# Optimization experiments

Measured on AMD Instinct MI355X. Metric: run time of the kernel, lower is better.

## Reference

```python
import jax, jax.numpy as jnp
import numpy as np

B, S, D, H = 2, 4096, 1024, 16
DH = D // H  # 64


def setup_inputs() -> dict:
    key = jax.random.key(0)
    ks = jax.random.split(key, 5)
    x = jax.random.normal(ks[0], (B, S, D), dtype=jnp.float32)
    scale = 1.0 / np.sqrt(D)
    Wq = jax.random.normal(ks[1], (D, D), dtype=jnp.float32) * scale
    Wk = jax.random.normal(ks[2], (D, D), dtype=jnp.float32) * scale
    Wv = jax.random.normal(ks[3], (D, D), dtype=jnp.float32) * scale
    Wo = jax.random.normal(ks[4], (D, D), dtype=jnp.float32) * scale
    bo = jnp.zeros((D,), dtype=jnp.float32)
    return {"x": x, "Wq": Wq, "Wk": Wk, "Wv": Wv, "Wo": Wo, "bo": bo}


def reference(x, Wq, Wk, Wv, Wo, bo):
    b, s, d = x.shape
    # QKV projections (no bias), split heads: [b, s, H, DH]
    q = (x @ Wq).reshape(b, s, H, DH)
    k = (x @ Wk).reshape(b, s, H, DH)
    v = (x @ Wv).reshape(b, s, H, DH)
    # scores: [b, H, s, s]
    scores = jnp.einsum("bqhd,bkhd->bhqk", q, k)
    # causal mask: upper triangle (j > i) set to -inf, then scale by sqrt(d_head)
    causal = jnp.triu(jnp.ones((s, s), dtype=bool), k=1)
    scores = jnp.where(causal, -jnp.inf, scores)
    weights = jax.nn.softmax(scores / jnp.sqrt(jnp.float32(DH)), axis=-1)
    # dropout rate is 0.0 -> identity
    ctx = jnp.einsum("bhqk,bkhd->bqhd", weights, v).reshape(b, s, d)
    return ctx @ Wo + bo
```

## Files before the change

### kernel.cpp

```cpp
#include <hip/hip_runtime.h>
#include <hip/hip_bf16.h>
#include <stdint.h>
#include <math.h>

#define BATCH 2
#define S_LEN 4096
#define DMODEL 1024
#define NH 16
#define DHEAD 64
#define MTOK (BATCH * S_LEN)

#define QSCALE 0.1803368801111793f

typedef unsigned short u16;
typedef __attribute__((ext_vector_type(8))) short bf16x8;
typedef __attribute__((ext_vector_type(4))) float f32x4;
typedef __attribute__((ext_vector_type(16))) float f32x16;
typedef __attribute__((ext_vector_type(4))) unsigned short u16x4;

__device__ __forceinline__ float b2f(u16 u) {
  union { unsigned int i; float f; } v; v.i = ((unsigned int)u) << 16; return v.f;
}
__device__ __forceinline__ u16 f2b(float f) {
  union { float f; unsigned int i; } v; v.f = f;
  unsigned int r = v.i + 0x7FFF + ((v.i >> 16) & 1);
  return (u16)(r >> 16);
}
__device__ __forceinline__ unsigned int pk2(float hi, float lo) {
  union { float f; unsigned int u; } a, b; a.f = hi; b.f = lo;
  return __builtin_amdgcn_perm(a.u, b.u, 0x07060302u);
}
__device__ __forceinline__ void pswap(unsigned int& a, unsigned int& b) {
  asm("v_permlane32_swap_b32 %0, %1" : "+v"(a), "+v"(b));
}

__device__ __forceinline__ void gl_lds16(const u16* g, u16* l) {
  __builtin_amdgcn_global_load_lds(
      (__attribute__((address_space(1))) void*)(u16*)g,
      (__attribute__((address_space(3))) void*)l, 16, 0, 0);
}

__global__ void detect_dtype(const unsigned int* __restrict__ x, int* __restrict__ flag) {
  __shared__ int cnt;
  if (threadIdx.x == 0) cnt = 0;
  __syncthreads();
  int c = 0;
  for (int i = threadIdx.x; i < 4096; i += 256) {
    unsigned int w = x[i];
    int e = (w >> 7) & 0xFF;
    if (e >= 100 && e <= 135) c++;
  }
  atomicAdd(&cnt, c);
  __syncthreads();
  if (threadIdx.x == 0) *flag = (cnt > 2048) ? 1 : 0;
}

__global__ void convert_x(const void* __restrict__ xin, u16* __restrict__ xc,
                          const int* __restrict__ flagp) {
  const int isb = *flagp;
  long e = ((long)blockIdx.x * 256 + threadIdx.x) * 4;
  if (isb) {
    *(uint2*)&xc[e] = *(const uint2*)((const u16*)xin + e);
  } else {
    float4 f = *(const float4*)((const float*)xin + e);
    xc[e + 0] = f2b(f.x);
    xc[e + 1] = f2b(f.y);
    xc[e + 2] = f2b(f.z);
    xc[e + 3] = f2b(f.w);
  }
}

__global__ void transpose4(const void* __restrict__ W0, const void* __restrict__ W1,
                           const void* __restrict__ W2, const void* __restrict__ W3,
                           u16* __restrict__ out, const int* __restrict__ flagp) {
  __shared__ u16 tile[32][33];
  const int isb = *flagp;
  int z = blockIdx.z;
  const void* W = (z == 0) ? W0 : (z == 1) ? W1 : (z == 2) ? W2 : W3;
  u16* o = out + (long)z * (DMODEL * DMODEL);
  int x = blockIdx.x * 32 + threadIdx.x;
  int y0 = blockIdx.y * 32;
  if (isb) {
    const u16* Wb = (const u16*)W;
#pragma unroll
    for (int i = 0; i < 32; i += 8)
      tile[threadIdx.y + i][threadIdx.x] = Wb[(long)(y0 + threadIdx.y + i) * DMODEL + x];
  } else {
    const float* Wf = (const float*)W;
#pragma unroll
    for (int i = 0; i < 32; i += 8)
      tile[threadIdx.y + i][threadIdx.x] = f2b(Wf[(long)(y0 + threadIdx.y + i) * DMODEL + x]);
  }
  __syncthreads();
  int x2 = blockIdx.y * 32 + threadIdx.x;
  int y2 = blockIdx.x * 32;
#pragma unroll
  for (int i = 0; i < 32; i += 8)
    o[(long)(y2 + threadIdx.y + i) * DMODEL + x2] = tile[threadIdx.x][threadIdx.y + i];
}

#define BM3 128
#define BN3 256
#define BK3 32
#define NT3 (DMODEL / BK3)
#define BUF3 12288

#define VM6 asm volatile("s_waitcnt vmcnt(6)" ::: "memory")
#define VM0 asm volatile("s_waitcnt vmcnt(0)" ::: "memory")
#define BARX do { asm volatile("" ::: "memory"); __builtin_amdgcn_s_barrier(); \
                  asm volatile("" ::: "memory"); } while (0)

#define STAGE3(t_, dst_)                                                          \
  do {                                                                            \
    const u16* a_ = pA + (t_) * BK3;                                              \
    const u16* b_ = pB + (t_) * BK3;                                              \
    u16* ad_ = (dst_) + w * 1024;                                                 \
    u16* bd_ = (dst_) + 4096 + w * 2048;                                          \
    gl_lds16(a_, ad_);                                                            \
    gl_lds16(a_ + 16 * DMODEL, ad_ + 512);                                        \
    gl_lds16(b_, bd_);                                                            \
    gl_lds16(b_ + 16 * DMODEL, bd_ + 512);                                        \
    gl_lds16(b_ + 32 * DMODEL, bd_ + 1024);                                       \
    gl_lds16(b_ + 48 * DMODEL, bd_ + 1536);                                       \
  } while (0)

#define GEMM_CORE5(A_, Bt_, NX_)                                                  \
  __shared__ __align__(16) u16 lds[3 * BUF3];                                     \
  const int tid = threadIdx.x;                                                    \
  const int w = tid >> 6;                                                         \
  const int lane = tid & 63;                                                      \
  const int nwg = (int)gridDim.x;                                                 \
  const int wg = (int)blockIdx.x;                                                 \
  const int swz = (wg & 7) * (nwg >> 3) + (wg >> 3);                              \
  const int m0 = (swz / (NX_)) * BM3;                                             \
  const int n0 = (swz % (NX_)) * BN3;                                             \
  const int wn = w * 64;                                                          \
  const int lc = lane & 15;                                                       \
  const int lq = lane >> 4;                                                       \
  const u16* pA = (A_) + (long)(m0 + w * 32 + (lane >> 2)) * DMODEL + (lane & 3) * 8; \
  const u16* pB = (Bt_) + (long)(n0 + w * 64 + (lane >> 2)) * DMODEL + (lane & 3) * 8; \
  f32x4 acc[8][4] = {};                                                           \
  STAGE3(0, lds);                                                                 \
  STAGE3(1, lds + BUF3);                                                          \
  for (int t = 0; t < NT3; ++t) {                                                 \
    if (t < NT3 - 1) { VM6; } else { VM0; }                                       \
    BARX;                                                                         \
    if (t + 2 < NT3) STAGE3(t + 2, lds + ((t + 2) % 3) * BUF3);                   \
    const u16* la = lds + (t % 3) * BUF3;                                         \
    const u16* lb = la + 4096;                                                    \
    bf16x8 af[8], bg[4];                                                          \
    _Pragma("unroll")                                                             \
    for (int j = 0; j < 4; ++j)                                                   \
      bg[j] = *(const bf16x8*)&lb[(wn + j * 16 + lc) * 32 + lq * 8];              \
    _Pragma("unroll")                                                             \
    for (int i = 0; i < 8; ++i)                                                   \
      af[i] = *(const bf16x8*)&la[(i * 16 + lc) * 32 + lq * 8];                   \
    __builtin_amdgcn_s_setprio(1);                                                \
    _Pragma("unroll")                                                             \
    for (int i = 0; i < 8; ++i)                                                   \
      _Pragma("unroll")                                                           \
      for (int j = 0; j < 4; ++j)                                                 \
        acc[i][j] = __builtin_amdgcn_mfma_f32_16x16x32_bf16(af[i], bg[j], acc[i][j], 0, 0, 0); \
    __builtin_amdgcn_s_setprio(0);                                                \
  }

__global__ __launch_bounds__(256, 2)
void gemm_qkv(const u16* __restrict__ A, const u16* __restrict__ Bt,
              u16* __restrict__ Qo, u16* __restrict__ Ko, u16* __restrict__ Vo) {
  GEMM_CORE5(A, Bt, 12)
#pragma unroll
  for (int i = 0; i < 8; ++i) {
#pragma unroll
    for (int j = 0; j < 4; ++j) {
      int n = n0 + wn + j * 16 + lc;
      int rgn = n >> 10;
      int nn = n & 1023;
      int h = nn >> 6, dh = nn & (DHEAD - 1);
      int m_base = m0 + i * 16 + lq * 4;
      int b = m_base >> 12, s0q = m_base & (S_LEN - 1);
      if (rgn == 2) {
        long idx_v = (((long)(b * NH + h)) * DHEAD + dh) * S_LEN + s0q;
        u16x4 vv;
#pragma unroll
        for (int r = 0; r < 4; ++r) vv[r] = f2b(acc[i][j][r]);
        *(u16x4*)&Vo[idx_v] = vv;
      } else {
        float sc = (rgn == 0) ? QSCALE : 1.0f;
        u16* dst = (rgn == 0) ? Qo : Ko;
#pragma unroll
        for (int r = 0; r < 4; ++r) {
          long idx_r = (((long)(b * NH + h)) * S_LEN + s0q + r) * DHEAD + dh;
          dst[idx_r] = f2b(acc[i][j][r] * sc);
        }
      }
    }
  }
}

__global__ __launch_bounds__(256, 2)
void gemm_out(const u16* __restrict__ A, const u16* __restrict__ Bt,
              const void* __restrict__ bias, void* __restrict__ C,
              const int* __restrict__ flagp) {
  GEMM_CORE5(A, Bt, 4)
  const int isb = *flagp;
#pragma unroll
  for (int i = 0; i < 8; ++i) {
#pragma unroll
    for (int j = 0; j < 4; ++j) {
      int n = n0 + wn + j * 16 + lc;
      float bv = isb ? b2f(((const u16*)bias)[n]) : ((const float*)bias)[n];
#pragma unroll
      for (int r = 0; r < 4; ++r) {
        int m = m0 + i * 16 + lq * 4 + r;
        float v = acc[i][j][r] + bv;
        if (isb) ((u16*)C)[(long)m * DMODEL + n] = f2b(v);
        else     ((float*)C)[(long)m * DMODEL + n] = v;
      }
    }
  }
}

__global__ __launch_bounds__(256, 2)
void flash_attn(const u16* __restrict__ Q, const u16* __restrict__ K,
                const u16* __restrict__ Vt, u16* __restrict__ ctx) {
  __shared__ __align__(16) u16 lK[2][64 * 64];
  __shared__ __align__(16) u16 lV[2][64 * 64];

  const int tid = threadIdx.x;
  const int w = tid >> 6;
  const int lane = tid & 63;
  const int l31 = lane & 31;
  const int l5 = lane >> 5;

  const int hb = blockIdx.x;
  const int h = hb & (NH - 1);
  const int b = hb >> 4;
  const int qt = gridDim.y - 1 - (int)blockIdx.y;
  const int q0 = qt * 128;

  const int bh = b * NH + h;
  const u16* Qb = Q + (long)bh * S_LEN * DHEAD;
  const u16* Kb = K + (long)bh * S_LEN * DHEAD;
  const u16* Vb = Vt + (long)bh * DHEAD * S_LEN;

  const int qa = q0 + w * 32;
  const int myq = qa + l31;

  bf16x8 aq[4];
#pragma unroll
  for (int c = 0; c < 4; ++c)
    aq[c] = *(const bf16x8*)(Qb + (long)myq * DHEAD + c * 16 + l5 * 8);

  union OU { unsigned int wd[4]; bf16x8 v; } ones;
#pragma unroll
  for (int i = 0; i < 4; ++i) ones.wd[i] = 0x3F803F80u;

  const int srow = tid >> 2;
  const int sc0 = (tid & 3) * 2;
  const int sd0 = srow * 64 + ((sc0 ^ (srow & 7)) * 8);
  const int sd1 = srow * 64 + (((sc0 + 1) ^ (srow & 7)) * 8);
  const u16* kp = Kb + (long)srow * DHEAD + sc0 * 8;
  const u16* vp = Vb + (long)srow * S_LEN + sc0 * 8;

  const int kmax = q0 + 64;
  bf16x8 kr0 = *(const bf16x8*)kp;
  bf16x8 kr1 = *(const bf16x8*)(kp + 8);
  bf16x8 vr0 = *(const bf16x8*)vp;
  bf16x8 vr1 = *(const bf16x8*)(vp + 8);
  const u16* kpre = kp + 64 * DHEAD;
  const u16* vpre = vp + 64;

  f32x16 o0 = {}, o1 = {};
  f32x16 lacc = {};
  const int xsw = l31 & 7;

  int offK[4][2];
#pragma unroll
  for (int c = 0; c < 4; ++c) {
    const int ch = c * 2 + l5;
    offK[c][0] = l31 * 64 + ((ch ^ xsw) * 8);
    offK[c][1] = (32 + l31) * 64 + ((ch ^ xsw) * 8);
  }

  for (int k0 = 0; k0 <= kmax; k0 += 64) {
    const int bi = (k0 >> 6) & 1;
    u16* lk = lK[bi];
    u16* lv = lV[bi];
    *(bf16x8*)&lk[sd0] = kr0;
    *(bf16x8*)&lk[sd1] = kr1;
    *(bf16x8*)&lv[sd0] = vr0;
    *(bf16x8*)&lv[sd1] = vr1;
    __syncthreads();

    if (k0 + 64 <= kmax) {
      kr0 = *(const bf16x8*)kpre;
      kr1 = *(const bf16x8*)(kpre + 8);
      vr0 = *(const bf16x8*)vpre;
      vr1 = *(const bf16x8*)(vpre + 8);
      kpre += 64 * DHEAD;
      vpre += 64;
    }

    if (k0 <= qa + 31) {
      f32x16 s0 = {}, s1 = {};
      __builtin_amdgcn_s_setprio(1);
#pragma unroll
      for (int c = 0; c < 4; ++c) {
        bf16x8 ak0 = *(const bf16x8*)&lk[offK[c][0]];
        bf16x8 ak1 = *(const bf16x8*)&lk[offK[c][1]];
        s0 = __builtin_amdgcn_mfma_f32_32x32x16_bf16(ak0, aq[c], s0, 0, 0, 0);
        s1 = __builtin_amdgcn_mfma_f32_32x32x16_bf16(ak1, aq[c], s1, 0, 0, 0);
      }
      __builtin_amdgcn_s_setprio(0);

      const bool masked = (k0 + 63 > qa);
      union BPU { unsigned int wd[4]; bf16x8 v; };
      BPU bp[4];
#pragma unroll
      for (int ph = 0; ph < 2; ++ph) {
        const f32x16 sv = ph ? s1 : s0;
        float p[16];
#pragma unroll
        for (int rr = 0; rr < 16; ++rr) {
          float e = __builtin_amdgcn_exp2f(sv[rr]);
          if (masked) {
            int kv = k0 + ph * 32 + (rr & 3) + 8 * (rr >> 2) + 4 * l5;
            e = (kv > myq) ? 0.0f : e;
          }
          p[rr] = e;
        }
#pragma unroll
        for (int g = 0; g < 2; ++g) {
          unsigned int A0 = pk2(p[8 * g + 1], p[8 * g + 0]);
          unsigned int A1 = pk2(p[8 * g + 3], p[8 * g + 2]);
          unsigned int B0 = pk2(p[8 * g + 5], p[8 * g + 4]);
          unsigned int B1 = pk2(p[8 * g + 7], p[8 * g + 6]);
          pswap(A0, B0);
          pswap(A1, B1);
          const int kc = ph * 2 + g;
          bp[kc].wd[0] = A0; bp[kc].wd[1] = A1;
          bp[kc].wd[2] = B0; bp[kc].wd[3] = B1;
        }
      }

      __builtin_amdgcn_s_setprio(1);
#pragma unroll
      for (int kc = 0; kc < 4; ++kc) {
        bf16x8 av0 = *(const bf16x8*)&lv[offK[kc][0]];
        bf16x8 av1 = *(const bf16x8*)&lv[offK[kc][1]];
        o0 = __builtin_amdgcn_mfma_f32_32x32x16_bf16(av0, bp[kc].v, o0, 0, 0, 0);
        o1 = __builtin_amdgcn_mfma_f32_32x32x16_bf16(av1, bp[kc].v, o1, 0, 0, 0);
        lacc = __builtin_amdgcn_mfma_f32_32x32x16_bf16(ones.v, bp[kc].v, lacc, 0, 0, 0);
      }
      __builtin_amdgcn_s_setprio(0);
    }
  }

  float inv = 1.0f / lacc[0];

  u16* cp = ctx + ((long)(b * S_LEN + myq)) * DMODEL + h * DHEAD;
#pragma unroll
  for (int d32 = 0; d32 < 2; ++d32) {
    const f32x16 ov = d32 ? o1 : o0;
#pragma unroll
    for (int g = 0; g < 4; ++g) {
      u16x4 st;
#pragma unroll
      for (int r = 0; r < 4; ++r) st[r] = f2b(ov[4 * g + r] * inv);
      *(u16x4*)&cp[d32 * 32 + g * 8 + l5 * 4] = st;
    }
  }
}

extern "C" void kernel_launch(void* const* d_in, const int* in_sizes, int n_in,
                              void* d_out, int out_size, void* d_ws, size_t ws_size,
                              hipStream_t stream) {
  const void* x  = d_in[0];
  const void* Wq = d_in[1];
  const void* Wk = d_in[2];
  const void* Wv = d_in[3];
  const void* Wo = d_in[4];
  const void* bo = d_in[5];
  u16* ws = (u16*)d_ws;

  u16* wt  = ws;
  u16* wto = wt + 3145728;
  u16* Qb  = ws + 4194304;
  u16* Vtb = ws + 12582912;
  u16* xc  = ws + 20971520;
  u16* ctx = xc;
  int* flag = (int*)(ws + 29360128);
  u16* Kb  = (u16*)d_out;

  detect_dtype<<<1, 256, 0, stream>>>((const unsigned int*)x, flag);
  convert_x<<<8192, 256, 0, stream>>>(x, xc, flag);
  transpose4<<<dim3(32, 32, 4), dim3(32, 8), 0, stream>>>(Wq, Wk, Wv, Wo, wt, flag);

  gemm_qkv<<<dim3(12 * 64), 256, 0, stream>>>(xc, wt, Qb, Kb, Vtb);

  flash_attn<<<dim3(NH * BATCH, S_LEN / 128), 256, 0, stream>>>(Qb, Kb, Vtb, ctx);

  gemm_out<<<dim3(4 * 64), 256, 0, stream>>>(ctx, wto, bo, d_out, flag);
}
```

Baseline: 288.7 us.

## Load K/V tiles directly global-to-LDS with async loads in attention loop

Replaces the register-staged K/V prefetch (global load to VGPRs, then ds_write) with direct global-to-LDS loads (gl_lds16), keeping the swizzled layout by permuting the source chunk index. The next tile is issued into the other LDS buffer right after the barrier, and each iteration waits on vmcnt(0) before syncing. This is meant to save VGPRs and ds_write instructions, with the global loads overlapping compute. The cost is a full vmcnt wait per iteration, and correctness depends on the gl_lds16 helper and its per-wave LDS offset layout.

```diff
diff --git a/kernel.cpp b/kernel.cpp
--- a/kernel.cpp
+++ b/kernel.cpp
@@ -255,20 +255,19 @@
 #pragma unroll
   for (int i = 0; i < 4; ++i) ones.wd[i] = 0x3F803F80u;
 
-  const int srow = tid >> 2;
-  const int sc0 = (tid & 3) * 2;
-  const int sd0 = srow * 64 + ((sc0 ^ (srow & 7)) * 8);
-  const int sd1 = srow * 64 + (((sc0 + 1) ^ (srow & 7)) * 8);
-  const u16* kp = Kb + (long)srow * DHEAD + sc0 * 8;
-  const u16* vp = Vb + (long)srow * S_LEN + sc0 * 8;
+  const int srow = tid >> 3;
+  const int schk = (tid & 7) ^ (srow & 7);
+  const u16* kp = Kb + (long)srow * DHEAD + schk * 8;
+  const u16* vp = Vb + (long)srow * S_LEN + schk * 8;
+  u16* dK = (u16*)lK + w * 512;
+  u16* dV = (u16*)lV + w * 512;
 
   const int kmax = q0 + 64;
-  bf16x8 kr0 = *(const bf16x8*)kp;
-  bf16x8 kr1 = *(const bf16x8*)(kp + 8);
-  bf16x8 vr0 = *(const bf16x8*)vp;
-  bf16x8 vr1 = *(const bf16x8*)(vp + 8);
-  const u16* kpre = kp + 64 * DHEAD;
-  const u16* vpre = vp + 64;
+
+  gl_lds16(kp, dK);
+  gl_lds16(kp + 32 * DHEAD, dK + 2048);
+  gl_lds16(vp, dV);
+  gl_lds16(vp + 32 * S_LEN, dV + 2048);
 
   f32x16 o0 = {}, o1 = {};
   f32x16 lacc = {};
@@ -284,22 +283,21 @@
 
   for (int k0 = 0; k0 <= kmax; k0 += 64) {
     const int bi = (k0 >> 6) & 1;
-    u16* lk = lK[bi];
-    u16* lv = lV[bi];
-    *(bf16x8*)&lk[sd0] = kr0;
-    *(bf16x8*)&lk[sd1] = kr1;
-    *(bf16x8*)&lv[sd0] = vr0;
-    *(bf16x8*)&lv[sd1] = vr1;
+    asm volatile("s_waitcnt vmcnt(0)" ::: "memory");
     __syncthreads();
 
     if (k0 + 64 <= kmax) {
-      kr0 = *(const bf16x8*)kpre;
-      kr1 = *(const bf16x8*)(kpre + 8);
-      vr0 = *(const bf16x8*)vpre;
-      vr1 = *(const bf16x8*)(vpre + 8);
-      kpre += 64 * DHEAD;
-      vpre += 64;
+      const int bn = bi ^ 1;
+      const u16* kt = kp + (long)(k0 + 64) * DHEAD;
+      const u16* vt = vp + (k0 + 64);
+      gl_lds16(kt, dK + bn * 4096);
+      gl_lds16(kt + 32 * DHEAD, dK + bn * 4096 + 2048);
+      gl_lds16(vt, dV + bn * 4096);
+      gl_lds16(vt + 32 * S_LEN, dV + bn * 4096 + 2048);
     }
+
+    const u16* lk = (const u16*)lK + bi * 4096;
+    const u16* lv = (const u16*)lV + bi * 4096;
 
     if (k0 <= qa + 31) {
       f32x16 s0 = {}, s1 = {};
```

Result: slower. 304.4 us (+5.4%).
